# Performance work log

Hardware: AMD Instinct MI355X
Metric: run time of the kernel (lower is better)

Reference implementation:

```python
import jax, jax.numpy as jnp
import numpy as np

WINDOW = 11
SIGMA = 1.5
K1 = 0.01
K2 = 0.03
L = 1.0


def _gauss_kernel(dtype):
    coords = jnp.arange(WINDOW, dtype=dtype) - (WINDOW - 1) / 2.0
    g = jnp.exp(-coords ** 2 / (2.0 * SIGMA ** 2))
    g = g / g.sum()
    return jnp.outer(g, g)  # [k, k]


def setup_inputs() -> dict:
    key = jax.random.key(0)
    k1, k2 = jax.random.split(key)
    B, T, H, W = 8, 16, 256, 256
    return {
        "predicted": jax.random.normal(k1, (B, T, H, W, 1), dtype=jnp.float32),
        "target": jax.random.normal(k2, (B, T, H, W, 1), dtype=jnp.float32),
    }


def reference(predicted, target):
    B, T, H, W, C = predicted.shape
    dt = predicted.dtype
    eps = jnp.asarray(1e-6, dt)

    # valid mask: samples whose target sums to zero are excluded (weighted mean)
    valid = (jnp.sum(target, axis=(1, 2, 3, 4)) != 0).astype(dt)  # [B]

    # per-sample, per-channel min-max normalization over (T, H, W)
    def norm(x):
        mn = jnp.min(x, axis=(1, 2, 3), keepdims=True)
        mx = jnp.max(x, axis=(1, 2, 3), keepdims=True)
        return (x - mn) / jnp.maximum(mx - mn, eps)

    p = norm(predicted)
    t = norm(target)

    # batch all (B,T) single-channel images through one conv: NCHW with N = B*T
    img1 = t.reshape(B * T, 1, H, W)  # original uses target as img1
    img2 = p.reshape(B * T, 1, H, W)
    kern = _gauss_kernel(dt).reshape(1, 1, WINDOW, WINDOW)
    pad = WINDOW // 2

    def conv(x):
        return jax.lax.conv_general_dilated(x, kern, (1, 1), [(pad, pad), (pad, pad)])

    mu1 = conv(img1)
    mu2 = conv(img2)
    mu1_sq = mu1 * mu1
    mu2_sq = mu2 * mu2
    mu1_mu2 = mu1 * mu2
    sigma1_sq = jnp.maximum(conv(img1 * img1) - mu1_sq, eps)
    sigma2_sq = jnp.maximum(conv(img2 * img2) - mu2_sq, eps)
    sigma12 = conv(img1 * img2) - mu1_mu2

    C1 = (K1 * L) ** 2
    C2 = (K2 * L) ** 2
    C3 = C2 / 2.0
    root = jnp.sqrt(sigma1_sq * sigma2_sq)
    luminance = (2.0 * mu1_mu2 + C1) / (mu1_sq + mu2_sq + C1)
    contrast = (2.0 * root + C2) / (sigma1_sq + sigma2_sq + C2)
    structure = (sigma12 + C3) / (root + C3)
    ssim_map = luminance * contrast * structure  # [B*T, 1, H, W]

    # per-(b,t) pixel mean, then mean over T == mean over (T,H,W)
    ssim_per_sample = ssim_map.reshape(B, T, H, W).mean(axis=(1, 2, 3))  # [B]

    n_valid = jnp.maximum(jnp.sum(valid), jnp.asarray(1.0, dt))
    loss = jnp.sum((1.0 - ssim_per_sample) * valid) / n_valid
    return loss
```

## Files before the change

kernel.cpp:

```cpp
#include <hip/hip_runtime.h>
#include <math.h>

#define BB 8
#define TT 16
#define HH 256
#define WW 256
#define NPX (TT * HH * WW)
#define CROWS 32
#define NBLK (BB * TT * (HH / CROWS))

#define P_MINP 0
#define P_MAXP 512
#define P_MINT 1024
#define P_MAXT 1536
#define P_SUMT 2048
#define WS_S   2560
#define WS_CNT 2561

typedef float v2f __attribute__((ext_vector_type(2)));

#define G0 0.0010283776f
#define G1 0.0075987582f
#define G2 0.0360008014f
#define G3 0.1093606427f
#define G4 0.2130055745f
#define G5 0.2660117857f
#define GA_(k) ((k) == 0 || (k) == 10 ? G0 : (k) == 1 || (k) == 9 ? G1 \
              : (k) == 2 || (k) == 8 ? G2 : (k) == 3 || (k) == 7 ? G3 \
              : (k) == 4 || (k) == 6 ? G4 : G5)

__global__ __launch_bounds__(256) void k_reduce(const float* __restrict__ p,
                                                const float* __restrict__ t,
                                                float* __restrict__ wsf) {
  const int b = blockIdx.x >> 6;
  const size_t base = (size_t)b * NPX + (size_t)(blockIdx.x & 63) * (NPX / 64);
  const int tid = threadIdx.x;

  float mnp = 3.4e38f, mxp = -3.4e38f, mnt = 3.4e38f, mxt = -3.4e38f, st = 0.f;
  const float4* p4 = (const float4*)(p + base);
  const float4* t4 = (const float4*)(t + base);
#pragma unroll 4
  for (int it = 0; it < 16; ++it) {
    float4 a = p4[it * 256 + tid];
    float4 c = t4[it * 256 + tid];
    mnp = fminf(mnp, fminf(fminf(a.x, a.y), fminf(a.z, a.w)));
    mxp = fmaxf(mxp, fmaxf(fmaxf(a.x, a.y), fmaxf(a.z, a.w)));
    mnt = fminf(mnt, fminf(fminf(c.x, c.y), fminf(c.z, c.w)));
    mxt = fmaxf(mxt, fmaxf(fmaxf(c.x, c.y), fmaxf(c.z, c.w)));
    st += c.x + c.y + c.z + c.w;
  }
  for (int off = 32; off > 0; off >>= 1) {
    mnp = fminf(mnp, __shfl_down(mnp, off));
    mxp = fmaxf(mxp, __shfl_down(mxp, off));
    mnt = fminf(mnt, __shfl_down(mnt, off));
    mxt = fmaxf(mxt, __shfl_down(mxt, off));
    st += __shfl_down(st, off);
  }
  __shared__ float s_mnp[4], s_mxp[4], s_mnt[4], s_mxt[4], s_st[4];
  int wave = tid >> 6, lane = tid & 63;
  if (lane == 0) {
    s_mnp[wave] = mnp; s_mxp[wave] = mxp;
    s_mnt[wave] = mnt; s_mxt[wave] = mxt; s_st[wave] = st;
  }
  __syncthreads();
  if (tid == 0) {
    for (int w = 1; w < 4; ++w) {
      mnp = fminf(mnp, s_mnp[w]); mxp = fmaxf(mxp, s_mxp[w]);
      mnt = fminf(mnt, s_mnt[w]); mxt = fmaxf(mxt, s_mxt[w]);
      st += s_st[w];
    }
    wsf[P_MINP + blockIdx.x] = mnp;
    wsf[P_MAXP + blockIdx.x] = mxp;
    wsf[P_MINT + blockIdx.x] = mnt;
    wsf[P_MAXT + blockIdx.x] = mxt;
    wsf[P_SUMT + blockIdx.x] = st;
    if (blockIdx.x == 0) {
      wsf[WS_S] = 0.f;
      ((unsigned int*)wsf)[WS_CNT] = 0u;
    }
  }
}

#define STEP(J) do {                                                         \
    constexpr int jj = (J);                                                  \
    constexpr int buf = jj & 1;                                              \
    constexpr int slot = jj % 11;                                            \
    const bool in = (unsigned)(ystart + jj) < (unsigned)HH;                  \
    v2f nv;                                                                  \
    nv.x = in ? fmaf(tcur, ts, tb) : 0.f;                                    \
    nv.y = in ? fmaf(pcur, ps, pb) : 0.f;                                    \
    srow[buf][x + 5] = nv;                                                   \
    __syncthreads();                                                         \
    if constexpr (jj < 41) {                                                 \
      const int yn = min(max(ystart + jj + 1, 0), HH - 1);                   \
      tnxt = tptr[(size_t)yn * WW + x];                                      \
      pnxt = pptr[(size_t)yn * WW + x];                                      \
    }                                                                        \
    v2f hmu = {0.f, 0.f}, hsq = {0.f, 0.f};                                  \
    float htp = 0.f;                                                         \
    _Pragma("unroll")                                                        \
    for (int k = 0; k < 11; ++k) {                                           \
      v2f v = srow[buf][x + k];                                              \
      v2f g2 = {GA_(k), GA_(k)};                                             \
      v2f w = g2 * v;                                                        \
      hmu = hmu + w;                                                         \
      hsq = __builtin_elementwise_fma(w, v, hsq);                            \
      htp = fmaf(w.x, v.y, htp);                                             \
    }                                                                        \
    r_mu[slot] = hmu; r_sq[slot] = hsq; r_tp[slot] = htp;                    \
    if constexpr (jj >= 10) {                                                \
      v2f vmu = {0.f, 0.f}, vsq = {0.f, 0.f};                                \
      float vtp = 0.f;                                                       \
      _Pragma("unroll")                                                      \
      for (int k = 0; k < 11; ++k) {                                         \
        const int s = (jj + 1 + k) % 11;                                     \
        v2f g2 = {GA_(k), GA_(k)};                                           \
        vmu = __builtin_elementwise_fma(g2, r_mu[s], vmu);                   \
        vsq = __builtin_elementwise_fma(g2, r_sq[s], vsq);                   \
        vtp = fmaf(GA_(k), r_tp[s], vtp);                                    \
      }                                                                      \
      float m1 = vmu.x, m2 = vmu.y;                                          \
      float mu11 = m1 * m1, mu22 = m2 * m2, m12 = m1 * m2;                   \
      float s1 = fmaxf(vsq.x - mu11, 1e-6f);                                 \
      float s2 = fmaxf(vsq.y - mu22, 1e-6f);                                 \
      float s12 = vtp - m12;                                                 \
      float root = sqrtf(s1 * s2);                                           \
      float num = fmaf(2.f, m12, C1) * fmaf(2.f, root, C2) * (s12 + C3);     \
      float den = (mu11 + mu22 + C1) * (s1 + s2 + C2) * (root + C3);         \
      acc = fmaf(num, __builtin_amdgcn_rcpf(den), acc);                      \
    }                                                                        \
    tcur = tnxt; pcur = pnxt;                                                \
    __builtin_amdgcn_sched_barrier(0);                                       \
  } while (0)

__global__ __launch_bounds__(256, 4) void k_ssim(const float* __restrict__ pred,
                                                 const float* __restrict__ targ,
                                                 float* __restrict__ wsf,
                                                 float* __restrict__ out) {
  const int img = blockIdx.x >> 3;
  const int chunk = blockIdx.x & 7;
  const int b = img >> 4;
  const int x = threadIdx.x;
  const int y0 = chunk * CROWS;
  const float* tptr = targ + (size_t)img * (HH * WW);
  const float* pptr = pred + (size_t)img * (HH * WW);

  __shared__ float sprm[5];
  if (x < 64) {
    float mnp = wsf[P_MINP + b * 64 + x];
    float mxp = wsf[P_MAXP + b * 64 + x];
    float mnt = wsf[P_MINT + b * 64 + x];
    float mxt = wsf[P_MAXT + b * 64 + x];
    float st  = wsf[P_SUMT + b * 64 + x];
    for (int off = 32; off > 0; off >>= 1) {
      mnp = fminf(mnp, __shfl_down(mnp, off));
      mxp = fmaxf(mxp, __shfl_down(mxp, off));
      mnt = fminf(mnt, __shfl_down(mnt, off));
      mxt = fmaxf(mxt, __shfl_down(mxt, off));
      st += __shfl_down(st, off);
    }
    if (x == 0) {
      float psv = 1.f / fmaxf(mxp - mnp, 1e-6f);
      float tsv = 1.f / fmaxf(mxt - mnt, 1e-6f);
      sprm[0] = psv; sprm[1] = -mnp * psv;
      sprm[2] = tsv; sprm[3] = -mnt * tsv;
      sprm[4] = (st != 0.f) ? 1.f : 0.f;
    }
  }

  __shared__ v2f srow[2][WW + 12];
  if (x < 5) {
    v2f z = {0.f, 0.f};
    srow[0][x] = z; srow[1][x] = z;
    srow[0][WW + 5 + x] = z; srow[1][WW + 5 + x] = z;
  }
  __syncthreads();
  const float ps = sprm[0], pb = sprm[1], ts = sprm[2], tb = sprm[3];

  v2f r_mu[11], r_sq[11];
  float r_tp[11];
  float acc = 0.f;
  const int ystart = y0 - 5;
  const float C1 = 1e-4f, C2 = 9e-4f, C3 = 4.5e-4f;

  float tcur, pcur, tnxt = 0.f, pnxt = 0.f;
  {
    const int yc = min(max(ystart, 0), HH - 1);
    tcur = tptr[(size_t)yc * WW + x];
    pcur = pptr[(size_t)yc * WW + x];
  }

  STEP(0);  STEP(1);  STEP(2);  STEP(3);  STEP(4);  STEP(5);  STEP(6);
  STEP(7);  STEP(8);  STEP(9);  STEP(10); STEP(11); STEP(12); STEP(13);
  STEP(14); STEP(15); STEP(16); STEP(17); STEP(18); STEP(19); STEP(20);
  STEP(21); STEP(22); STEP(23); STEP(24); STEP(25); STEP(26); STEP(27);
  STEP(28); STEP(29); STEP(30); STEP(31); STEP(32); STEP(33); STEP(34);
  STEP(35); STEP(36); STEP(37); STEP(38); STEP(39); STEP(40); STEP(41);

  for (int off = 32; off > 0; off >>= 1) acc += __shfl_down(acc, off);
  __shared__ float sred[4];
  __shared__ unsigned int s_last;
  if ((x & 63) == 0) sred[x >> 6] = acc;
  __syncthreads();
  if (x == 0) {
    float v = sred[0] + sred[1] + sred[2] + sred[3];
    atomicAdd(&wsf[WS_S], v * sprm[4]);
    __threadfence();
    unsigned int old = atomicAdd(((unsigned int*)wsf) + WS_CNT, 1u);
    s_last = (old == (unsigned int)(NBLK - 1)) ? 1u : 0u;
  }
  __syncthreads();

  if (s_last && x < 64) {
    float sums[8];
#pragma unroll
    for (int bb = 0; bb < 8; ++bb) sums[bb] = wsf[P_SUMT + bb * 64 + x];
    for (int off = 32; off > 0; off >>= 1) {
#pragma unroll
      for (int bb = 0; bb < 8; ++bb) sums[bb] += __shfl_down(sums[bb], off);
    }
    if (x == 0) {
      __threadfence();
      float sv = 0.f;
#pragma unroll
      for (int bb = 0; bb < 8; ++bb) sv += (sums[bb] != 0.f) ? 1.f : 0.f;
      float S = atomicAdd(&wsf[WS_S], 0.f);
      out[0] = (sv - S * (1.f / (float)NPX)) / fmaxf(sv, 1.f);
    }
  }
}

extern "C" void kernel_launch(void* const* d_in, const int* in_sizes, int n_in,
                              void* d_out, int out_size, void* d_ws, size_t ws_size,
                              hipStream_t stream) {
  const float* pred = (const float*)d_in[0];
  const float* targ = (const float*)d_in[1];
  float* wsf = (float*)d_ws;
  float* out = (float*)d_out;

  hipLaunchKernelGGL(k_reduce, dim3(512), dim3(256), 0, stream, pred, targ, wsf);
  hipLaunchKernelGGL(k_ssim, dim3(NBLK), dim3(256), 0, stream, pred, targ, wsf, out);
}
```

Baseline: 151.6 us.

## Split SSIM row tiles per wavefront with halo to drop block-wide barriers

Each 64-lane wavefront now owns a 54-column strip plus a 5-column halo on each side, with its own double-buffered LDS row buffer. This removes the per-row __syncthreads across the whole block. The block grows from 256 to 320 threads, so halo lanes add redundant global loads and arithmetic (about 25% more lane work) in exchange for wave-local synchronisation only. Lanes outside the output range are masked out of the accumulation.

```diff
diff --git a/kernel.cpp b/kernel.cpp
--- a/kernel.cpp
+++ b/kernel.cpp
@@ -86,21 +86,21 @@
     constexpr int buf = jj & 1;                                              \
     constexpr int slot = jj % 11;                                            \
     const bool in = (unsigned)(ystart + jj) < (unsigned)HH;                  \
+    const bool sel = in && colok;                                            \
     v2f nv;                                                                  \
-    nv.x = in ? fmaf(tcur, ts, tb) : 0.f;                                    \
-    nv.y = in ? fmaf(pcur, ps, pb) : 0.f;                                    \
-    srow[buf][x + 5] = nv;                                                   \
-    __syncthreads();                                                         \
+    nv.x = sel ? fmaf(tcur, ts, tb) : 0.f;                                   \
+    nv.y = sel ? fmaf(pcur, ps, pb) : 0.f;                                   \
+    swav[wid][buf][lane + 5] = nv;                                           \
     if constexpr (jj < 41) {                                                 \
       const int yn = min(max(ystart + jj + 1, 0), HH - 1);                   \
-      tnxt = tptr[(size_t)yn * WW + x];                                      \
-      pnxt = pptr[(size_t)yn * WW + x];                                      \
+      tnxt = tptr[(size_t)yn * WW + colc];                                   \
+      pnxt = pptr[(size_t)yn * WW + colc];                                   \
     }                                                                        \
     v2f hmu = {0.f, 0.f}, hsq = {0.f, 0.f};                                  \
     float htp = 0.f;                                                         \
     _Pragma("unroll")                                                        \
     for (int k = 0; k < 11; ++k) {                                           \
-      v2f v = srow[buf][x + k];                                              \
+      v2f v = swav[wid][buf][lane + k];                                      \
       v2f g2 = {GA_(k), GA_(k)};                                             \
       v2f w = g2 * v;                                                        \
       hmu = hmu + w;                                                         \
@@ -127,13 +127,13 @@
       float root = sqrtf(s1 * s2);                                           \
       float num = fmaf(2.f, m12, C1) * fmaf(2.f, root, C2) * (s12 + C3);     \
       float den = (mu11 + mu22 + C1) * (s1 + s2 + C2) * (root + C3);         \
-      acc = fmaf(num, __builtin_amdgcn_rcpf(den), acc);                      \
+      if (colv) acc = fmaf(num, __builtin_amdgcn_rcpf(den), acc);            \
     }                                                                        \
     tcur = tnxt; pcur = pnxt;                                                \
     __builtin_amdgcn_sched_barrier(0);                                       \
   } while (0)
 
-__global__ __launch_bounds__(256, 4) void k_ssim(const float* __restrict__ pred,
+__global__ __launch_bounds__(320, 5) void k_ssim(const float* __restrict__ pred,
                                                  const float* __restrict__ targ,
                                                  float* __restrict__ wsf,
                                                  float* __restrict__ out) {
@@ -141,6 +141,7 @@
   const int chunk = blockIdx.x & 7;
   const int b = img >> 4;
   const int x = threadIdx.x;
+  const int wid = x >> 6, lane = x & 63;
   const int y0 = chunk * CROWS;
   const float* tptr = targ + (size_t)img * (HH * WW);
   const float* pptr = pred + (size_t)img * (HH * WW);
@@ -168,14 +169,14 @@
     }
   }
 
-  __shared__ v2f srow[2][WW + 12];
-  if (x < 5) {
-    v2f z = {0.f, 0.f};
-    srow[0][x] = z; srow[1][x] = z;
-    srow[0][WW + 5 + x] = z; srow[1][WW + 5 + x] = z;
-  }
+  __shared__ v2f swav[5][2][74];
   __syncthreads();
   const float ps = sprm[0], pb = sprm[1], ts = sprm[2], tb = sprm[3];
+
+  const int col = wid * 54 - 5 + lane;
+  const bool colok = (col >= 0) && (col < WW);
+  const int colc = min(max(col, 0), WW - 1);
+  const bool colv = (lane >= 5) && (lane <= 58) && (col < WW);
 
   v2f r_mu[11], r_sq[11];
   float r_tp[11];
@@ -186,8 +187,8 @@
   float tcur, pcur, tnxt = 0.f, pnxt = 0.f;
   {
     const int yc = min(max(ystart, 0), HH - 1);
-    tcur = tptr[(size_t)yc * WW + x];
-    pcur = pptr[(size_t)yc * WW + x];
+    tcur = tptr[(size_t)yc * WW + colc];
+    pcur = pptr[(size_t)yc * WW + colc];
   }
 
   STEP(0);  STEP(1);  STEP(2);  STEP(3);  STEP(4);  STEP(5);  STEP(6);
@@ -198,12 +199,12 @@
   STEP(35); STEP(36); STEP(37); STEP(38); STEP(39); STEP(40); STEP(41);
 
   for (int off = 32; off > 0; off >>= 1) acc += __shfl_down(acc, off);
-  __shared__ float sred[4];
+  __shared__ float sred[5];
   __shared__ unsigned int s_last;
-  if ((x & 63) == 0) sred[x >> 6] = acc;
+  if (lane == 0) sred[wid] = acc;
   __syncthreads();
   if (x == 0) {
-    float v = sred[0] + sred[1] + sred[2] + sred[3];
+    float v = sred[0] + sred[1] + sred[2] + sred[3] + sred[4];
     atomicAdd(&wsf[WS_S], v * sprm[4]);
     __threadfence();
     unsigned int old = atomicAdd(((unsigned int*)wsf) + WS_CNT, 1u);
@@ -239,5 +240,5 @@
   float* out = (float*)d_out;
 
   hipLaunchKernelGGL(k_reduce, dim3(512), dim3(256), 0, stream, pred, targ, wsf);
-  hipLaunchKernelGGL(k_ssim, dim3(NBLK), dim3(256), 0, stream, pred, targ, wsf, out);
+  hipLaunchKernelGGL(k_ssim, dim3(NBLK), dim3(320), 0, stream, pred, targ, wsf, out);
 }
```

Measured after the change: 167.6 us. +10.6%, slower.
